# Kernel optimization log

Measured on AMD Instinct MI355X. Metric: run time of the kernel, lower is better.

## Reference

```python
import jax, jax.numpy as jnp
import numpy as np

B, T, F, H, C = 1024, 64, 256, 1024, 2


def setup_inputs() -> dict:
    key = jax.random.key(0)
    ks = jax.random.split(key, 16)
    s = 1.0 / np.sqrt(H)
    return {
        "X": jax.random.normal(ks[0], (B, T, F), jnp.float32),
        "missing_mask": (jax.random.uniform(ks[1], (B, T, F)) > 0.3).astype(jnp.float32),
        "deltas": jax.random.uniform(ks[2], (B, T, F), jnp.float32) * 5.0,
        "empirical_mean": jax.random.normal(ks[3], (B, F), jnp.float32),
        "X_filledLOCF": jax.random.normal(ks[4], (B, T, F), jnp.float32),
        # TemporalDecay h: full linear F->H
        "w_gh": jax.random.normal(ks[5], (H, F), jnp.float32) * 0.02,
        "b_gh": jnp.zeros((H,), jnp.float32),
        # TemporalDecay x: diagonal (W masked by identity) -> vector of size F
        "w_gx": jax.random.normal(ks[6], (F,), jnp.float32) * 0.02,
        "b_gx": jnp.zeros((F,), jnp.float32),
        # GRUCell: input size 2F+H, hidden H
        "w_ih": jax.random.uniform(ks[7], (3 * H, 2 * F + H), jnp.float32, -s, s),
        "w_hh": jax.random.uniform(ks[8], (3 * H, H), jnp.float32, -s, s),
        "b_ih": jax.random.uniform(ks[9], (3 * H,), jnp.float32, -s, s),
        "b_hh": jax.random.uniform(ks[10], (3 * H,), jnp.float32, -s, s),
        # classifier H -> C
        "w_cls": jax.random.normal(ks[11], (C, H), jnp.float32) * 0.02,
        "b_cls": jnp.zeros((C,), jnp.float32),
    }


def _grud_forward(X, missing_mask, deltas, empirical_mean, X_filledLOCF,
                  w_gh, b_gh, w_gx, b_gx, w_ih, w_hh, b_ih, b_hh, w_cls, b_cls):
    # time-major for scan: [T, B, F]
    Xt = jnp.swapaxes(X, 0, 1)
    Mt = jnp.swapaxes(missing_mask, 0, 1)
    Dt = jnp.swapaxes(deltas, 0, 1)
    Lt = jnp.swapaxes(X_filledLOCF, 0, 1)

    def step(h, xs):
        x, m, d, x_locf = xs
        # TemporalDecay: gamma = exp(-relu(W d + b))
        gamma_h = jnp.exp(-jax.nn.relu(d @ w_gh.T + b_gh))        # [B, H]
        gamma_x = jnp.exp(-jax.nn.relu(d * w_gx + b_gx))          # [B, F] (diag)
        h = h * gamma_h
        x_h = gamma_x * x_locf + (1.0 - gamma_x) * empirical_mean
        x_replaced = m * x + (1.0 - m) * x_h
        inp = jnp.concatenate([x_replaced, h, m], axis=1)         # [B, 2F+H]
        # GRUCell
        gi = inp @ w_ih.T + b_ih                                   # [B, 3H]
        gh = h @ w_hh.T + b_hh                                     # [B, 3H]
        i_r, i_z, i_n = jnp.split(gi, 3, axis=1)
        h_r, h_z, h_n = jnp.split(gh, 3, axis=1)
        r = jax.nn.sigmoid(i_r + h_r)
        z = jax.nn.sigmoid(i_z + h_z)
        n = jnp.tanh(i_n + r * h_n)
        h_new = (1.0 - z) * n + z * h
        return h_new, None

    h0 = jnp.zeros((X.shape[0], w_hh.shape[1]), X.dtype)
    h_final, _ = jax.lax.scan(step, h0, (Xt, Mt, Dt, Lt))
    logits = h_final @ w_cls.T + b_cls
    return jax.nn.softmax(logits, axis=1)


def reference(X, missing_mask, deltas, empirical_mean, X_filledLOCF,
              w_gh, b_gh, w_gx, b_gx, w_ih, w_hh, b_ih, b_hh, w_cls, b_cls):
    return _grud_forward(X, missing_mask, deltas, empirical_mean, X_filledLOCF,
                         w_gh, b_gh, w_gx, b_gx, w_ih, w_hh, b_ih, b_hh, w_cls, b_cls)
```

## Files before the change

kernel.cpp:

```cpp
#include <hip/hip_runtime.h>

using bf16   = __bf16;
using bf16x8 = __bf16 __attribute__((ext_vector_type(8)));
using f32x4  = float  __attribute__((ext_vector_type(4)));
using i32x4  = int    __attribute__((ext_vector_type(4)));


__device__ __forceinline__ float sigm(float x) { return 1.f / (1.f + __expf(-x)); }
__device__ __forceinline__ float tanh_fast(float x) {
  float e = __expf(2.f * x);
  return 1.f - 2.f / (e + 1.f);
}

#define GLL16(gsrc, ldst)                                                              \
  __builtin_amdgcn_global_load_lds((const __attribute__((address_space(1))) void*)(gsrc), \
                                   (__attribute__((address_space(3))) void*)(ldst), 16, 0, 0)

__global__ void prep_kernel(const float* __restrict__ X, const float* __restrict__ Msk,
                            const float* __restrict__ D, const float* __restrict__ Mean,
                            const float* __restrict__ L, const float* __restrict__ w_gx,
                            const float* __restrict__ b_gx,
                            bf16* __restrict__ XRs, bf16* __restrict__ Dbfs,
                            int c, int nsl) {
  int i = blockIdx.x * 256 + threadIdx.x;
  if (i >= (nsl << 18)) return;
  int f = i & 255, b = (i >> 8) & 1023, tl = i >> 18;
  int t = c * 16 + tl;
  size_t g = ((size_t)b << 14) + ((size_t)t << 8) + f;
  float d = D[g];
  int fs = f ^ ((b & 7) << 3);
  int row = tl * 1024 + b;
  Dbfs[(size_t)row * 256 + fs] = (bf16)d;
  float gx = __expf(-fmaxf(d * w_gx[f] + b_gx[f], 0.f));
  float xh = gx * L[g] + (1.f - gx) * Mean[(size_t)b * 256 + f];
  float m  = Msk[g];
  float xr = m * X[g] + (1.f - m) * xh;
  if (tl < 16) {
    size_t xo = (size_t)row * 512;
    XRs[xo + fs]       = (bf16)xr;
    XRs[xo + 256 + fs] = (bf16)m;
  }
}

__global__ void wprep_kernel(const float* __restrict__ w_ih, const float* __restrict__ w_hh,
                             const float* __restrict__ b_ih, const float* __restrict__ b_hh,
                             const float* __restrict__ w_gh,
                             char* __restrict__ WcH3, bf16* __restrict__ WcX3,
                             bf16* __restrict__ Wgs, float* __restrict__ bias4) {
  int i = blockIdx.x * 256 + threadIdx.x;
  if (i < 4194304) {
    int nb = i >> 17;
    int rem = i & 131071;
    int kt = rem >> 14;
    int r2 = rem & 16383;
    int nl = r2 >> 7, bb = r2 & 127;
    int cc = bb >> 4, e = bb & 15;
    int gg = nl >> 5, j = nb * 32 + (nl & 31);
    int k = kt * 128 + ((cc ^ (nl & 7)) << 4) + e;
    float v;
    if (gg == 3) v = w_hh[(size_t)(2048 + j) * 1024 + k];
    else {
      int rr = gg * 1024 + j;
      v = w_ih[(size_t)rr * 1536 + 256 + k];
      if (gg < 2) v += w_hh[(size_t)rr * 1024 + k];
    }
    float sc = (gg >= 2) ? 4096.f : 2048.f;
    int wq = __float2int_rn(v * sc);
    wq = wq > 127 ? 127 : (wq < -127 ? -127 : wq);
    WcH3[i] = (char)wq;
  } else if (i < 5767168) {
    int q = i - 4194304;
    int blk = q >> 13;
    int nb = blk >> 3, kt = blk & 7;
    int r = q & 8191;
    int nl = r >> 6, cc = (r >> 3) & 7, e = r & 7;
    int gg = nb >> 3;
    int j  = (nb & 7) * 128 + nl;
    int rr = gg * 1024 + j;
    int k = kt * 64 + ((cc ^ (nl & 7)) << 3) + e;
    float v = (k < 256) ? w_ih[(size_t)rr * 1536 + k]
                        : w_ih[(size_t)rr * 1536 + 1280 + (k - 256)];
    WcX3[q] = (bf16)v;
  } else if (i < 6029312) {
    int q = i - 5767168;
    int blk = q >> 13;
    int nb = blk >> 2, kt = blk & 3;
    int r = q & 8191;
    int nl = r >> 6, cc = (r >> 3) & 7, e = r & 7;
    int n = nb * 128 + nl;
    int k = kt * 64 + ((cc ^ (nl & 7)) << 3) + e;
    Wgs[q] = (bf16)w_gh[(size_t)n * 256 + k];
  } else if (i < 6033408) {
    int q = i - 6029312;
    int gg = q >> 10, j = q & 1023;
    float v;
    if (gg == 0)      v = b_ih[j] + b_hh[j];
    else if (gg == 1) v = b_ih[1024 + j] + b_hh[1024 + j];
    else if (gg == 2) v = b_ih[2048 + j];
    else              v = b_hh[2048 + j];
    bias4[q] = v;
  }
}

__global__ __launch_bounds__(256) void combo_kernel(
    const bf16* __restrict__ XRs, const bf16* __restrict__ WcX3,
    bf16* __restrict__ Gi, int gxblocks,
    const bf16* __restrict__ Dbfs, const bf16* __restrict__ Wgs,
    const float* __restrict__ b_gh, bf16* __restrict__ GH, int gmblocks) {
  __shared__ char smem[65536];
  char* As = smem;
  char* Bs = smem + 32768;
  int bid = blockIdx.x;
  int tid = threadIdx.x, lane = tid & 63, wid = tid >> 6;
  int wr = wid >> 1, wc = wid & 1;

  if (bid < gxblocks) {
    int cpx = gxblocks >> 3;
    int wg = (bid & 7) * cpx + (bid >> 3);
    int nb = wg % 24, mb = wg / 24;

    const bf16* aA = XRs + ((size_t)(mb * 128 + wid * 8 + (lane >> 3))) * 512 + (lane & 7) * 8;
    const bf16* aB = WcX3 + (size_t)nb * 8 * 8192 + wid * 512 + lane * 8;

    f32x4 acc[4][4];
#pragma unroll
    for (int a = 0; a < 4; ++a)
#pragma unroll
      for (int b = 0; b < 4; ++b)
#pragma unroll
        for (int q = 0; q < 4; ++q) acc[a][b][q] = 0.f;

#define GX_STAGE(buf, kt)                                                         \
  do {                                                                            \
    _Pragma("unroll")                                                             \
    for (int q = 0; q < 4; ++q)                                                   \
      GLL16(aA + q * (32 * 512) + (kt) * 64, As + (buf) * 16384 + (q * 4 + wid) * 1024); \
    _Pragma("unroll")                                                             \
    for (int q = 0; q < 4; ++q)                                                   \
      GLL16(aB + (size_t)(kt) * 8192 + q * 2048, Bs + (buf) * 16384 + (q * 4 + wid) * 1024); \
  } while (0)

    GX_STAGE(0, 0);
    __syncthreads();
    for (int kt = 0; kt < 8; ++kt) {
      const int cur = kt & 1;
      if (kt < 7) GX_STAGE(cur ^ 1, kt + 1);
#pragma unroll
      for (int kk = 0; kk < 2; ++kk) {
        int kb = kk * 64 + ((lane >> 4) << 4);
        bf16x8 af[4], bfr[4];
#pragma unroll
        for (int mf = 0; mf < 4; ++mf) {
          int row = wr * 64 + mf * 16 + (lane & 15);
          af[mf] = *(const bf16x8*)(As + cur * 16384 + (((row * 128 + kb)) ^ ((row & 7) << 4)));
        }
#pragma unroll
        for (int nf = 0; nf < 4; ++nf) {
          int nl = wc * 64 + nf * 16 + (lane & 15);
          bfr[nf] = *(const bf16x8*)(Bs + cur * 16384 + (((nl * 128 + kb)) ^ ((nl & 7) << 4)));
        }
#pragma unroll
        for (int mf = 0; mf < 4; ++mf)
#pragma unroll
          for (int nf = 0; nf < 4; ++nf)
            acc[mf][nf] = __builtin_amdgcn_mfma_f32_16x16x32_bf16(af[mf], bfr[nf], acc[mf][nf], 0, 0, 0);
      }
      __syncthreads();
    }
    char* ep = smem;
#pragma unroll
    for (int nf = 0; nf < 4; ++nf) {
      int col = wc * 64 + nf * 16 + (lane & 15);
#pragma unroll
      for (int mf = 0; mf < 4; ++mf)
#pragma unroll
        for (int reg = 0; reg < 4; ++reg) {
          int row = wr * 64 + mf * 16 + ((lane >> 4) << 2) + reg;
          int cph = ((col >> 3) ^ (((row >> 2) & 3) << 2));
          *(bf16*)(ep + row * 256 + (cph << 4) + (col & 7) * 2) = (bf16)acc[mf][nf][reg];
        }
    }
    __syncthreads();
    {
      int sl = mb >> 3, mbl = mb & 7;
      bf16* plane = Gi + (size_t)sl * 3145728 + (size_t)(nb >> 3) * 1048576 + (nb & 7) * 128;
#pragma unroll
      for (int p = 0; p < 8; ++p) {
        int idx = p * 256 + tid;
        int row = idx >> 4, c = idx & 15;
        int cph = c ^ (((row >> 2) & 3) << 2);
        bf16x8 v = *(const bf16x8*)(ep + row * 256 + (cph << 4));
        __builtin_nontemporal_store(v, (bf16x8*)(plane + (size_t)(mbl * 128 + row) * 1024 + c * 8));
      }
    }
    return;
  }

  {
    int lbid = bid - gxblocks;
    int cpx = gmblocks >> 3;
    int wg = (lbid & 7) * cpx + (lbid >> 3);
    int nb = wg & 7, mb = wg >> 3;

    const bf16* aA = Dbfs + ((size_t)(mb * 128 + wid * 8 + (lane >> 3))) * 256 + (lane & 7) * 8;
    const bf16* aB = Wgs + (size_t)nb * 4 * 8192 + wid * 512 + lane * 8;

    f32x4 acc[4][4];
#pragma unroll
    for (int a = 0; a < 4; ++a)
#pragma unroll
      for (int b = 0; b < 4; ++b)
#pragma unroll
        for (int q = 0; q < 4; ++q) acc[a][b][q] = 0.f;

#define GM_STAGE(buf, kt)                                                         \
  do {                                                                            \
    _Pragma("unroll")                                                             \
    for (int q = 0; q < 4; ++q)                                                   \
      GLL16(aA + q * (32 * 256) + (kt) * 64, As + (buf) * 16384 + (q * 4 + wid) * 1024); \
    _Pragma("unroll")                                                             \
    for (int q = 0; q < 4; ++q)                                                   \
      GLL16(aB + (size_t)(kt) * 8192 + q * 2048, Bs + (buf) * 16384 + (q * 4 + wid) * 1024); \
  } while (0)

    GM_STAGE(0, 0);
    __syncthreads();
    for (int kt = 0; kt < 4; ++kt) {
      const int cur = kt & 1;
      if (kt < 3) GM_STAGE(cur ^ 1, kt + 1);
#pragma unroll
      for (int kk = 0; kk < 2; ++kk) {
        int kb = kk * 64 + ((lane >> 4) << 4);
        bf16x8 af[4], bfr[4];
#pragma unroll
        for (int mf = 0; mf < 4; ++mf) {
          int row = wr * 64 + mf * 16 + (lane & 15);
          af[mf] = *(const bf16x8*)(As + cur * 16384 + (((row * 128 + kb)) ^ ((row & 7) << 4)));
        }
#pragma unroll
        for (int nf = 0; nf < 4; ++nf) {
          int nl = wc * 64 + nf * 16 + (lane & 15);
          bfr[nf] = *(const bf16x8*)(Bs + cur * 16384 + (((nl * 128 + kb)) ^ ((nl & 7) << 4)));
        }
#pragma unroll
        for (int mf = 0; mf < 4; ++mf)
#pragma unroll
          for (int nf = 0; nf < 4; ++nf)
            acc[mf][nf] = __builtin_amdgcn_mfma_f32_16x16x32_bf16(af[mf], bfr[nf], acc[mf][nf], 0, 0, 0);
      }
      __syncthreads();
    }
    char* ep = smem;
#pragma unroll
    for (int nf = 0; nf < 4; ++nf) {
      int col = wc * 64 + nf * 16 + (lane & 15);
      float bg = b_gh[nb * 128 + col];
#pragma unroll
      for (int mf = 0; mf < 4; ++mf)
#pragma unroll
        for (int reg = 0; reg < 4; ++reg) {
          int row = wr * 64 + mf * 16 + ((lane >> 4) << 2) + reg;
          int cph = ((col >> 3) ^ (((row >> 2) & 3) << 2));
          *(bf16*)(ep + row * 256 + (cph << 4) + (col & 7) * 2) =
              (bf16)__expf(-fmaxf(acc[mf][nf][reg] + bg, 0.f));
        }
    }
    __syncthreads();
#pragma unroll
    for (int p = 0; p < 8; ++p) {
      int idx = p * 256 + tid;
      int row = idx >> 4, c = idx & 15;
      int cph = c ^ (((row >> 2) & 3) << 2);
      bf16x8 v = *(const bf16x8*)(ep + row * 256 + (cph << 4));
      __builtin_nontemporal_store(v, (bf16x8*)(GH + (size_t)(mb * 128 + row) * 1024 + nb * 128 + c * 8));
    }
  }
}

__global__ __launch_bounds__(512, 4) void step_kernel(
    const char* __restrict__ hbs, const bf16* __restrict__ hf,
    const char* __restrict__ WcH3, const float* __restrict__ bias4,
    const bf16* __restrict__ gi, const bf16* __restrict__ gh_next, int is_last,
    bf16* __restrict__ hf_next, char* __restrict__ hbs_next) {
  __shared__ char smem[49152];
  int tid = threadIdx.x, lane = tid & 63, wid = tid >> 6;
  int wr = wid >> 1, wc = wid & 1;
  int wg = ((blockIdx.x & 7) << 6) + (blockIdx.x >> 3);
  int mb = wg & 15, nb = wg >> 4;

  const char* aA = hbs + (size_t)(mb * 64 + (tid >> 3)) * 1024 + (tid & 7) * 16;
  const char* aB = WcH3 + (size_t)nb * 131072 + (tid >> 3) * 128 + (tid & 7) * 16;

  int j = nb * 32 + wc * 16 + (lane & 15);
  bf16  grv[4], gzv[4], gnv[4], ghv[4], hfv[4];
#pragma unroll
  for (int reg = 0; reg < 4; ++reg) {
    int brow = mb * 64 + wr * 16 + ((lane >> 4) << 2) + reg;
    size_t hb_ = (size_t)brow * 1024 + j;
    grv[reg] = gi[hb_];
    gzv[reg] = gi[1048576 + hb_];
    gnv[reg] = gi[2097152 + hb_];
    ghv[reg] = gh_next[hb_];
    hfv[reg] = hf[hb_];
  }

  i32x4 acc[4];
#pragma unroll
  for (int b = 0; b < 4; ++b)
#pragma unroll
    for (int q = 0; q < 4; ++q) acc[b][q] = 0;

#define ST_STAGE(buf, kt)                                                            \
  do {                                                                               \
    GLL16(aA + (kt) * 128,            smem + (buf) * 8192 + wid * 1024);             \
    GLL16(aB + (kt) * 16384,          smem + 16384 + (buf) * 16384 + wid * 1024);    \
    GLL16(aB + (kt) * 16384 + 8192,   smem + 16384 + (buf) * 16384 + 8192 + wid * 1024); \
  } while (0)

  ST_STAGE(0, 0);
  __syncthreads();
  for (int kt = 0; kt < 8; ++kt) {
    const int cur = kt & 1;
    if (kt < 7) ST_STAGE(cur ^ 1, kt + 1);
    const char* Ab = smem + cur * 8192;
    const char* Bb = smem + 16384 + cur * 16384;
#pragma unroll
    for (int kk = 0; kk < 2; ++kk) {
      int kb = kk * 64 + ((lane >> 4) << 4);
      int row = wr * 16 + (lane & 15);
      i32x4 af = *(const i32x4*)(Ab + ((row * 128 + (kb ^ ((row & 7) << 4)))));
      i32x4 bfr[4];
#pragma unroll
      for (int g = 0; g < 4; ++g) {
        int nl = g * 32 + wc * 16 + (lane & 15);
        bfr[g] = *(const i32x4*)(Bb + ((nl * 128 + (kb ^ ((nl & 7) << 4)))));
      }
#pragma unroll
      for (int g = 0; g < 4; ++g)
        acc[g] = __builtin_amdgcn_mfma_i32_16x16x64_i8(af, bfr[g], acc[g], 0, 0, 0);
    }
    __syncthreads();
  }

  const float ISC_RZ = 3.814697265625e-06f;
  const float ISC_N  = 1.9073486328125e-06f;
  float br = bias4[j], bz = bias4[1024 + j], bn = bias4[2048 + j], bh = bias4[3072 + j];
#pragma unroll
  for (int reg = 0; reg < 4; ++reg) {
    int brow = mb * 64 + wr * 16 + ((lane >> 4) << 2) + reg;
    float pr  = (float)acc[0][reg] * ISC_RZ + (float)grv[reg] + br;
    float pz  = (float)acc[1][reg] * ISC_RZ + (float)gzv[reg] + bz;
    float pin = (float)acc[2][reg] * ISC_N  + (float)gnv[reg] + bn;
    float phn = (float)acc[3][reg] * ISC_N  + bh;
    float r = sigm(pr), z = sigm(pz);
    float nn = tanh_fast(pin + r * phn);
    float hnew = (1.f - z) * nn + z * (float)hfv[reg];
    float gam = is_last ? 1.f : (float)ghv[reg];
    float hd = hnew * gam;
    hf_next[(size_t)brow * 1024 + j] = (bf16)hd;
    int hi8 = __float2int_rn(hd * 128.f);
    hi8 = hi8 > 127 ? 127 : (hi8 < -127 ? -127 : hi8);
    hbs_next[(size_t)brow * 1024 + (j ^ ((brow & 7) << 4))] = (char)hi8;
  }
}

__global__ void cls_kernel(const bf16* __restrict__ h, const float* __restrict__ w_cls,
                           const float* __restrict__ b_cls, float* __restrict__ out) {
  int wid = threadIdx.x >> 6, lane = threadIdx.x & 63;
  int b = blockIdx.x * 4 + wid;
  const bf16* hb = h + (size_t)b * 1024;
  float a0 = 0.f, a1 = 0.f;
#pragma unroll
  for (int e = 0; e < 16; ++e) {
    int i = e * 64 + lane;
    float hv = (float)hb[i];
    a0 += hv * w_cls[i];
    a1 += hv * w_cls[1024 + i];
  }
  for (int off = 32; off; off >>= 1) {
    a0 += __shfl_down(a0, off);
    a1 += __shfl_down(a1, off);
  }
  if (lane == 0) {
    float l0 = a0 + b_cls[0], l1 = a1 + b_cls[1];
    float mx = fmaxf(l0, l1);
    float e0 = __expf(l0 - mx), e1 = __expf(l1 - mx);
    float s = e0 + e1;
    out[b * 2]     = e0 / s;
    out[b * 2 + 1] = e1 / s;
  }
}

extern "C" void kernel_launch(void* const* d_in, const int* in_sizes, int n_in,
                              void* d_out, int out_size, void* d_ws, size_t ws_size,
                              hipStream_t stream) {
  const float* X     = (const float*)d_in[0];
  const float* Msk   = (const float*)d_in[1];
  const float* D     = (const float*)d_in[2];
  const float* Mean  = (const float*)d_in[3];
  const float* L     = (const float*)d_in[4];
  const float* w_gh  = (const float*)d_in[5];
  const float* b_gh  = (const float*)d_in[6];
  const float* w_gx  = (const float*)d_in[7];
  const float* b_gx  = (const float*)d_in[8];
  const float* w_ih  = (const float*)d_in[9];
  const float* w_hh  = (const float*)d_in[10];
  const float* b_ih  = (const float*)d_in[11];
  const float* b_hh  = (const float*)d_in[12];
  const float* w_cls = (const float*)d_in[13];
  const float* b_cls = (const float*)d_in[14];

  char* w = (char*)d_ws;
  bf16*  XRs   = (bf16*)(w);
  bf16*  Dbfs  = (bf16*)(w + 16777216);
  bf16*  GH    = (bf16*)(w + 25690112);
  bf16*  WcX3  = (bf16*)(w + 61341696);
  char*  WcH3  = (char*)(w + 65536000);
  bf16*  Wgs   = (bf16*)(w + 73924608);
  float* bias4 = (float*)(w + 74448896);
  bf16*  hf0   = (bf16*)(w + 74465280);
  bf16*  hf1   = (bf16*)(w + 78659584);
  char*  hb0   = (char*)(w + 82853888);
  char*  hb1   = (char*)(w + 84951040);
  bf16*  Gi    = (bf16*)(w + 87048192);

  size_t base = 87048192;
  int GCH = 16;
  while (GCH > 1 && base + (size_t)GCH * 6291456ull > ws_size) GCH >>= 1;

  bf16*  hfp[2] = {hf0, hf1};
  char*  hbp[2] = {hb0, hb1};

  hipMemsetAsync(hf0, 0, 2097152, stream);
  hipMemsetAsync(hb0, 0, 1048576, stream);
  wprep_kernel<<<23568, 256, 0, stream>>>(w_ih, w_hh, b_ih, b_hh, w_gh, WcH3, WcX3, Wgs, bias4);

  int t = 0;
  for (int c = 0; c < 4; ++c) {
    int nsl = (c < 3) ? 17 : 16;
    prep_kernel<<<nsl * 1024, 256, 0, stream>>>(X, Msk, D, Mean, L, w_gx, b_gx, XRs, Dbfs, c, nsl);
    for (int sub = 0; sub < 16 / GCH; ++sub) {
      int gxblocks = GCH * 192;
      int nsl2 = (sub == 0) ? nsl : 0;
      combo_kernel<<<gxblocks + nsl2 * 64, 256, 0, stream>>>(
          XRs + (size_t)sub * GCH * 524288, WcX3, Gi, gxblocks,
          Dbfs, Wgs, b_gh, GH, nsl2 * 64);
      for (int tl2 = 0; tl2 < GCH; ++tl2, ++t) {
        int tl = sub * GCH + tl2;
        int cur = t & 1, nxt = cur ^ 1;
        step_kernel<<<512, 512, 0, stream>>>(
            hbp[cur], hfp[cur], WcH3, bias4,
            Gi + (size_t)tl2 * 3145728, GH + (size_t)(tl + 1) * 1048576,
            (t == 63) ? 1 : 0, hfp[nxt], hbp[nxt]);
      }
    }
  }
  cls_kernel<<<256, 256, 0, stream>>>(hfp[0], w_cls, b_cls, (float*)d_out);
}
```

Before: 1.125 ms.

## Fuse next-chunk input prep into combo kernel with double-buffered prep outputs

Removes the separate per-chunk prep_kernel launch and runs the next chunk's input preprocessing as extra blocks inside combo_kernel. XRs/Dbfs are double-buffered so prep of chunk c+1 can run while the current chunk's GEMMs read chunk c. The GCH fallback for small workspace is dropped, so it now always assumes 16 timesteps of Gi fit in the workspace. The gain depends on whether the prep blocks hide behind the GEMM blocks or just add tail work.

```diff
diff --git a/kernel.cpp b/kernel.cpp
--- a/kernel.cpp
+++ b/kernel.cpp
@@ -16,14 +16,11 @@
   __builtin_amdgcn_global_load_lds((const __attribute__((address_space(1))) void*)(gsrc), \
                                    (__attribute__((address_space(3))) void*)(ldst), 16, 0, 0)
 
-__global__ void prep_kernel(const float* __restrict__ X, const float* __restrict__ Msk,
-                            const float* __restrict__ D, const float* __restrict__ Mean,
-                            const float* __restrict__ L, const float* __restrict__ w_gx,
-                            const float* __restrict__ b_gx,
-                            bf16* __restrict__ XRs, bf16* __restrict__ Dbfs,
-                            int c, int nsl) {
-  int i = blockIdx.x * 256 + threadIdx.x;
-  if (i >= (nsl << 18)) return;
+__device__ __forceinline__ void prep_one(int i, int c,
+    const float* __restrict__ X, const float* __restrict__ Msk,
+    const float* __restrict__ D, const float* __restrict__ Mean,
+    const float* __restrict__ L, const float* __restrict__ w_gx,
+    const float* __restrict__ b_gx, bf16* __restrict__ XRs, bf16* __restrict__ Dbfs) {
   int f = i & 255, b = (i >> 8) & 1023, tl = i >> 18;
   int t = c * 16 + tl;
   size_t g = ((size_t)b << 14) + ((size_t)t << 8) + f;
@@ -40,6 +37,17 @@
     XRs[xo + fs]       = (bf16)xr;
     XRs[xo + 256 + fs] = (bf16)m;
   }
+}
+
+__global__ void prep_kernel(const float* __restrict__ X, const float* __restrict__ Msk,
+                            const float* __restrict__ D, const float* __restrict__ Mean,
+                            const float* __restrict__ L, const float* __restrict__ w_gx,
+                            const float* __restrict__ b_gx,
+                            bf16* __restrict__ XRs, bf16* __restrict__ Dbfs,
+                            int c, int nsl) {
+  int i = blockIdx.x * 256 + threadIdx.x;
+  if (i >= (nsl << 18)) return;
+  prep_one(i, c, X, Msk, D, Mean, L, w_gx, b_gx, XRs, Dbfs);
 }
 
 __global__ void wprep_kernel(const float* __restrict__ w_ih, const float* __restrict__ w_hh,
@@ -106,7 +114,12 @@
     const bf16* __restrict__ XRs, const bf16* __restrict__ WcX3,
     bf16* __restrict__ Gi, int gxblocks,
     const bf16* __restrict__ Dbfs, const bf16* __restrict__ Wgs,
-    const float* __restrict__ b_gh, bf16* __restrict__ GH, int gmblocks) {
+    const float* __restrict__ b_gh, bf16* __restrict__ GH, int gmblocks,
+    const float* __restrict__ X, const float* __restrict__ Msk,
+    const float* __restrict__ D, const float* __restrict__ Mean,
+    const float* __restrict__ L, const float* __restrict__ w_gx,
+    const float* __restrict__ b_gx,
+    bf16* __restrict__ XRsN, bf16* __restrict__ DbfsN, int pc, int npsl) {
   __shared__ char smem[65536];
   char* As = smem;
   char* Bs = smem + 32768;
@@ -196,7 +209,7 @@
     return;
   }
 
-  {
+  if (bid < gxblocks + gmblocks) {
     int lbid = bid - gxblocks;
     int cpx = gmblocks >> 3;
     int wg = (lbid & 7) * cpx + (lbid >> 3);
@@ -274,6 +287,14 @@
       bf16x8 v = *(const bf16x8*)(ep + row * 256 + (cph << 4));
       __builtin_nontemporal_store(v, (bf16x8*)(GH + (size_t)(mb * 128 + row) * 1024 + nb * 128 + c * 8));
     }
+    return;
+  }
+
+  {
+    int r2 = bid - gxblocks - gmblocks;
+    int total = npsl << 18;
+    for (int i = r2 * 256 + tid; i < total; i += 1024 * 256)
+      prep_one(i, pc, X, Msk, D, Mean, L, w_gx, b_gx, XRsN, DbfsN);
   }
 }
 
@@ -411,48 +432,40 @@
   const float* b_cls = (const float*)d_in[14];
 
   char* w = (char*)d_ws;
-  bf16*  XRs   = (bf16*)(w);
-  bf16*  Dbfs  = (bf16*)(w + 16777216);
-  bf16*  GH    = (bf16*)(w + 25690112);
-  bf16*  WcX3  = (bf16*)(w + 61341696);
-  char*  WcH3  = (char*)(w + 65536000);
-  bf16*  Wgs   = (bf16*)(w + 73924608);
-  float* bias4 = (float*)(w + 74448896);
-  bf16*  hf0   = (bf16*)(w + 74465280);
-  bf16*  hf1   = (bf16*)(w + 78659584);
-  char*  hb0   = (char*)(w + 82853888);
-  char*  hb1   = (char*)(w + 84951040);
-  bf16*  Gi    = (bf16*)(w + 87048192);
-
-  size_t base = 87048192;
-  int GCH = 16;
-  while (GCH > 1 && base + (size_t)GCH * 6291456ull > ws_size) GCH >>= 1;
-
-  bf16*  hfp[2] = {hf0, hf1};
-  char*  hbp[2] = {hb0, hb1};
-
-  hipMemsetAsync(hf0, 0, 2097152, stream);
-  hipMemsetAsync(hb0, 0, 1048576, stream);
+  bf16*  XRp[2]  = {(bf16*)(w), (bf16*)(w + 16777216)};
+  bf16*  Dbp[2]  = {(bf16*)(w + 33554432), (bf16*)(w + 42467328)};
+  bf16*  GH      = (bf16*)(w + 51380224);
+  bf16*  WcX3    = (bf16*)(w + 87031808);
+  char*  WcH3    = (char*)(w + 90177536);
+  bf16*  Wgs     = (bf16*)(w + 94371840);
+  float* bias4   = (float*)(w + 94896128);
+  bf16*  hfp[2]  = {(bf16*)(w + 94912512), (bf16*)(w + 97009664)};
+  char*  hbp[2]  = {(char*)(w + 99106816), (char*)(w + 100155392)};
+  bf16*  Gi      = (bf16*)(w + 101203968);
+
+  hipMemsetAsync(hfp[0], 0, 2097152, stream);
+  hipMemsetAsync(hbp[0], 0, 1048576, stream);
   wprep_kernel<<<23568, 256, 0, stream>>>(w_ih, w_hh, b_ih, b_hh, w_gh, WcH3, WcX3, Wgs, bias4);
+
+  prep_kernel<<<17 * 1024, 256, 0, stream>>>(X, Msk, D, Mean, L, w_gx, b_gx, XRp[0], Dbp[0], 0, 17);
 
   int t = 0;
   for (int c = 0; c < 4; ++c) {
-    int nsl = (c < 3) ? 17 : 16;
-    prep_kernel<<<nsl * 1024, 256, 0, stream>>>(X, Msk, D, Mean, L, w_gx, b_gx, XRs, Dbfs, c, nsl);
-    for (int sub = 0; sub < 16 / GCH; ++sub) {
-      int gxblocks = GCH * 192;
-      int nsl2 = (sub == 0) ? nsl : 0;
-      combo_kernel<<<gxblocks + nsl2 * 64, 256, 0, stream>>>(
-          XRs + (size_t)sub * GCH * 524288, WcX3, Gi, gxblocks,
-          Dbfs, Wgs, b_gh, GH, nsl2 * 64);
-      for (int tl2 = 0; tl2 < GCH; ++tl2, ++t) {
-        int tl = sub * GCH + tl2;
-        int cur = t & 1, nxt = cur ^ 1;
-        step_kernel<<<512, 512, 0, stream>>>(
-            hbp[cur], hfp[cur], WcH3, bias4,
-            Gi + (size_t)tl2 * 3145728, GH + (size_t)(tl + 1) * 1048576,
-            (t == 63) ? 1 : 0, hfp[nxt], hbp[nxt]);
-      }
+    int pr = c & 1, pn = pr ^ 1;
+    int nsl  = (c < 3) ? 17 : 16;
+    int npsl = (c < 3) ? ((c + 1 < 3) ? 17 : 16) : 0;
+    int gxblocks = 3072, gmblocks = nsl * 64;
+    int grid = gxblocks + gmblocks + ((npsl > 0) ? 1024 : 0);
+    combo_kernel<<<grid, 256, 0, stream>>>(
+        XRp[pr], WcX3, Gi, gxblocks,
+        Dbp[pr], Wgs, b_gh, GH, gmblocks,
+        X, Msk, D, Mean, L, w_gx, b_gx, XRp[pn], Dbp[pn], c + 1, npsl);
+    for (int tl = 0; tl < 16; ++tl, ++t) {
+      int cur = t & 1, nxt = cur ^ 1;
+      step_kernel<<<512, 512, 0, stream>>>(
+          hbp[cur], hfp[cur], WcH3, bias4,
+          Gi + (size_t)tl * 3145728, GH + (size_t)(tl + 1) * 1048576,
+          (t == 63) ? 1 : 0, hfp[nxt], hbp[nxt]);
     }
   }
   cls_kernel<<<256, 256, 0, stream>>>(hfp[0], w_cls, b_cls, (float*)d_out);
```

After: 1.171 ms. 4.1% more time.
